# Kernel tuning notes

Hardware: AMD Instinct MI355X
Metric: run time of the kernel (lower is better)

Reference implementation:

```python
import jax, jax.numpy as jnp
import numpy as np

EPS = 1e-12  # torch F.normalize default eps


def _l2_normalize(x):
    # normalize along last dim, matching F.normalize(dim=2)
    norm = jnp.linalg.norm(x, axis=-1, keepdims=True)
    return x / jnp.maximum(norm, EPS)


def _poly_kernel_mean(a, b):
    # mean over (B,C,C) of squared inner products along T.
    # Original does broadcast (B,1,C,T)*(B,C,1,T) then sum; einsum is the
    # efficient batched-matmul form of the same math.
    g = jnp.einsum('bct,bdt->bcd', a, b)  # (B,C,C)
    return jnp.mean(g * g)


def setup_inputs() -> dict:
    key = jax.random.key(0)
    k1, k2 = jax.random.split(key)
    B, C, T = 16, 128, 16384
    f_s = jax.random.normal(k1, (B, C, T), dtype=jnp.float32)
    f_t = jax.random.normal(k2, (B, C, T), dtype=jnp.float32)
    return {"f_s": f_s, "f_t": f_t}


def reference(f_s, f_t):
    # equal T -> no interpolation branch; view(B,C,-1) is identity for 3D
    s = _l2_normalize(f_s)
    t = _l2_normalize(f_t)
    loss = (jax.lax.stop_gradient(_poly_kernel_mean(t, t))
            + _poly_kernel_mean(s, s)
            - 2.0 * _poly_kernel_mean(s, t))
    return loss
```

## Files before the change

kernel.cpp:

```cpp
#include <hip/hip_runtime.h>
#include <hip/hip_bf16.h>

#define BATCH  16
#define CCH    128
#define TDIM   16384
#define MROWS  256
#define NCHUNK 16
#define KC     (TDIM / NCHUNK)
#define BK     32
#define NSTEP  (KC / BK)
#define LDSP   40
#define GRAM   (MROWS * MROWS)

#define WS_NORMS 0
#define WS_DIAG  4096
#define WS_BODY  (4096 + 65536)

typedef __attribute__((ext_vector_type(8))) short bf16x8;
typedef __attribute__((ext_vector_type(4))) float f32x4;
typedef __attribute__((ext_vector_type(8))) unsigned short u16x8;

__device__ __forceinline__ unsigned short f2bf(float x) {
  unsigned int u = __float_as_uint(x);
  u += 0x7fffu + ((u >> 16) & 1u);
  return (unsigned short)(u >> 16);
}

__global__ __launch_bounds__(512, 2) void gram_kernel(
    const float* __restrict__ fs, const float* __restrict__ ft,
    float* __restrict__ outp, float* __restrict__ diagp, int atomic_mode)
{
  __shared__ __attribute__((aligned(16))) unsigned short sm[2][MROWS][LDSP];

  const int tid   = threadIdx.x;
  const int bidx  = blockIdx.x;
  const int b     = bidx / NCHUNK;
  const int chunk = bidx - b * NCHUNK;
  const int kbase = chunk * KC;

  const int lane = tid & 63;
  const int w    = tid >> 6;
  const int wr   = w & 3;
  const int wc   = w >> 2;
  const int lhi  = lane >> 4;
  const int llo  = lane & 15;
  const int koff = lhi * 8;

  const int srow = tid >> 1;
  const int half = tid & 1;
  const float* rp = ((srow < CCH)
      ? (fs + (size_t)(b * CCH + srow) * TDIM)
      : (ft + (size_t)(b * CCH + (srow - CCH)) * TDIM))
      + kbase + half * 16;

  f32x4 acc[4][8];
  #pragma unroll
  for (int i = 0; i < 4; ++i)
    #pragma unroll
    for (int j = 0; j < 8; ++j)
      acc[i][j] = (f32x4){0.f, 0.f, 0.f, 0.f};

  {
    f32x4 v0 = *(const f32x4*)(rp + 0);
    f32x4 v1 = *(const f32x4*)(rp + 4);
    f32x4 v2 = *(const f32x4*)(rp + 8);
    f32x4 v3 = *(const f32x4*)(rp + 12);
    u16x8 pa, pb;
    pa[0]=f2bf(v0.x); pa[1]=f2bf(v0.y); pa[2]=f2bf(v0.z); pa[3]=f2bf(v0.w);
    pa[4]=f2bf(v1.x); pa[5]=f2bf(v1.y); pa[6]=f2bf(v1.z); pa[7]=f2bf(v1.w);
    pb[0]=f2bf(v2.x); pb[1]=f2bf(v2.y); pb[2]=f2bf(v2.z); pb[3]=f2bf(v2.w);
    pb[4]=f2bf(v3.x); pb[5]=f2bf(v3.y); pb[6]=f2bf(v3.z); pb[7]=f2bf(v3.w);
    *(u16x8*)&sm[0][srow][half * 16]     = pa;
    *(u16x8*)&sm[0][srow][half * 16 + 8] = pb;
  }
  f32x4 p[2][4];
  #pragma unroll
  for (int k = 0; k < 4; ++k)
    p[1][k] = *(const f32x4*)(rp + 1 * BK + k * 4);
  __syncthreads();

  #pragma unroll 2
  for (int s = 0; s < NSTEP; ++s) {
    const int par = s & 1;
    if (s + 2 < NSTEP) {
      #pragma unroll
      for (int k = 0; k < 4; ++k)
        p[par][k] = *(const f32x4*)(rp + (s + 2) * BK + k * 4);
    }
    {
      bf16x8 af[4], bfr[8];
      #pragma unroll
      for (int i = 0; i < 4; ++i)
        af[i] = *(const bf16x8*)&sm[par][wr * 64 + i * 16 + llo][koff];
      #pragma unroll
      for (int j = 0; j < 8; ++j)
        bfr[j] = *(const bf16x8*)&sm[par][wc * 128 + j * 16 + llo][koff];
      #pragma unroll
      for (int i = 0; i < 4; ++i)
        #pragma unroll
        for (int j = 0; j < 8; ++j)
          acc[i][j] = __builtin_amdgcn_mfma_f32_16x16x32_bf16(af[i], bfr[j], acc[i][j], 0, 0, 0);
    }
    if (s + 1 < NSTEP) {
      u16x8 pa, pb;
      pa[0]=f2bf(p[par^1][0].x); pa[1]=f2bf(p[par^1][0].y); pa[2]=f2bf(p[par^1][0].z); pa[3]=f2bf(p[par^1][0].w);
      pa[4]=f2bf(p[par^1][1].x); pa[5]=f2bf(p[par^1][1].y); pa[6]=f2bf(p[par^1][1].z); pa[7]=f2bf(p[par^1][1].w);
      pb[0]=f2bf(p[par^1][2].x); pb[1]=f2bf(p[par^1][2].y); pb[2]=f2bf(p[par^1][2].z); pb[3]=f2bf(p[par^1][2].w);
      pb[4]=f2bf(p[par^1][3].x); pb[5]=f2bf(p[par^1][3].y); pb[6]=f2bf(p[par^1][3].z); pb[7]=f2bf(p[par^1][3].w);
      *(u16x8*)&sm[par ^ 1][srow][half * 16]     = pa;
      *(u16x8*)&sm[par ^ 1][srow][half * 16 + 8] = pb;
    }
    __syncthreads();
  }

  if (atomic_mode) {
    float* out = outp + (size_t)b * GRAM;
    #pragma unroll
    for (int i = 0; i < 4; ++i) {
      int row0 = wr * 64 + i * 16 + lhi * 4;
      #pragma unroll
      for (int j = 0; j < 8; ++j) {
        int col = wc * 128 + j * 16 + llo;
        #pragma unroll
        for (int r = 0; r < 4; ++r)
          atomicAdd(&out[(size_t)(row0 + r) * MROWS + col], acc[i][j][r]);
      }
    }
    if ((wr >> 1) == wc && (llo >> 2) == lhi) {
      #pragma unroll
      for (int i = 0; i < 4; ++i) {
        float dv = (wr & 1) ? acc[i][4 + i][llo & 3] : acc[i][i][llo & 3];
        atomicAdd(&diagp[b * MROWS + wr * 64 + i * 16 + llo], dv);
      }
    }
  } else {
    float* out = outp + (size_t)bidx * GRAM;
    #pragma unroll
    for (int i = 0; i < 4; ++i) {
      int row0 = wr * 64 + i * 16 + lhi * 4;
      #pragma unroll
      for (int j = 0; j < 8; ++j) {
        int col = wc * 128 + j * 16 + llo;
        #pragma unroll
        for (int r = 0; r < 4; ++r)
          out[(size_t)(row0 + r) * MROWS + col] = acc[i][j][r];
      }
    }
    if ((wr >> 1) == wc && (llo >> 2) == lhi) {
      #pragma unroll
      for (int i = 0; i < 4; ++i) {
        float dv = (wr & 1) ? acc[i][4 + i][llo & 3] : acc[i][i][llo & 3];
        diagp[bidx * MROWS + wr * 64 + i * 16 + llo] = dv;
      }
    }
  }
}

__global__ __launch_bounds__(256) void norms_kernel(
    const float* __restrict__ diagp, float* __restrict__ norms, int nchunk)
{
  int b = blockIdx.x;
  int d = threadIdx.x;
  float g = 0.f;
  for (int c = 0; c < nchunk; ++c)
    g += diagp[(b * nchunk + c) * MROWS + d];
  float n = sqrtf(fmaxf(g, 0.f));
  n = fmaxf(n, 1e-12f);
  norms[b * MROWS + d] = 1.0f / n;
}

__global__ __launch_bounds__(256) void loss_kernel(
    const float* __restrict__ body, const float* __restrict__ norms,
    float* __restrict__ out, int nchunk)
{
  int flat = blockIdx.x * 1024 + threadIdx.x * 4;
  int b    = flat >> 16;
  int e    = flat & 65535;
  const float* nb = norms + b * MROWS;

  f32x4 g = (f32x4){0.f, 0.f, 0.f, 0.f};
  const float* src = body + (size_t)b * nchunk * GRAM + e;
  #pragma unroll 4
  for (int c = 0; c < nchunk; ++c) {
    f32x4 v = *(const f32x4*)(src + (size_t)c * GRAM);
    g.x += v.x; g.y += v.y; g.z += v.z; g.w += v.w;
  }
  int i  = e >> 8;
  int j0 = e & 255;
  float ri = nb[i];
  f32x4 rj = *(const f32x4*)(nb + j0);
  float si = (i < CCH) ? 1.f : -1.f;
  float accl = 0.f;
  #pragma unroll
  for (int q = 0; q < 4; ++q) {
    int j = j0 + q;
    float gh = g[q] * ri * rj[q];
    float sgn = ((j < CCH) ? 1.f : -1.f) * si;
    accl += sgn * gh * gh;
  }
  #pragma unroll
  for (int off = 32; off > 0; off >>= 1)
    accl += __shfl_down(accl, off, 64);
  __shared__ float red[4];
  if ((threadIdx.x & 63) == 0) red[threadIdx.x >> 6] = accl;
  __syncthreads();
  if (threadIdx.x == 0) {
    float t = red[0] + red[1] + red[2] + red[3];
    atomicAdd(out, t * (1.0f / (float)(BATCH * CCH * CCH)));
  }
}

extern "C" void kernel_launch(void* const* d_in, const int* in_sizes, int n_in,
                              void* d_out, int out_size, void* d_ws, size_t ws_size,
                              hipStream_t stream) {
  const float* fs = (const float*)d_in[0];
  const float* ft = (const float*)d_in[1];
  float* out   = (float*)d_out;
  float* wsf   = (float*)d_ws;
  float* norms = wsf + WS_NORMS;
  float* diagp = wsf + WS_DIAG;
  float* body  = wsf + WS_BODY;

  const size_t need_partials =
      (size_t)(WS_BODY + (size_t)BATCH * NCHUNK * GRAM) * sizeof(float);
  const int atomic_mode = (ws_size >= need_partials) ? 0 : 1;
  const int nchunk = atomic_mode ? 1 : NCHUNK;

  (void)hipMemsetAsync(d_out, 0, sizeof(float), stream);
  if (atomic_mode) {
    (void)hipMemsetAsync(diagp, 0,
        (size_t)(65536 + (size_t)BATCH * GRAM) * sizeof(float), stream);
  }

  gram_kernel<<<dim3(BATCH * NCHUNK), dim3(512), 0, stream>>>(fs, ft, body, diagp, atomic_mode);
  norms_kernel<<<dim3(BATCH), dim3(256), 0, stream>>>(diagp, norms, nchunk);
  loss_kernel<<<dim3(1024), dim3(256), 0, stream>>>(body, norms, out, nchunk);
}
```

Measured before the change: 332.4 us.

## Triple-buffer LDS staging with two global loads in flight in gram kernel

Replaces the double-buffered K loop with a three-stage pipeline: three LDS buffers and three register staging sets. This lets two future K-steps' global loads be outstanding while the current step's MFMAs run. The loop is manually rotated over the three buffers, with an explicit tail and one barrier per step. The B-fragment loads are also split into two halves to lower peak register use. The aim is to hide HBM latency, since there is only one block per CU. The cost is more LDS per block and extra staging registers, which could spill or limit residency.

```diff
diff --git a/kernel.cpp b/kernel.cpp
--- a/kernel.cpp
+++ b/kernel.cpp
@@ -30,7 +30,7 @@
     const float* __restrict__ fs, const float* __restrict__ ft,
     float* __restrict__ outp, float* __restrict__ diagp, int atomic_mode)
 {
-  __shared__ __attribute__((aligned(16))) unsigned short sm[2][MROWS][LDSP];
+  __shared__ __attribute__((aligned(16))) unsigned short sm[3][MROWS][LDSP];
 
   const int tid   = threadIdx.x;
   const int bidx  = blockIdx.x;
@@ -60,58 +60,69 @@
     for (int j = 0; j < 8; ++j)
       acc[i][j] = (f32x4){0.f, 0.f, 0.f, 0.f};
 
-  {
-    f32x4 v0 = *(const f32x4*)(rp + 0);
-    f32x4 v1 = *(const f32x4*)(rp + 4);
-    f32x4 v2 = *(const f32x4*)(rp + 8);
-    f32x4 v3 = *(const f32x4*)(rp + 12);
-    u16x8 pa, pb;
-    pa[0]=f2bf(v0.x); pa[1]=f2bf(v0.y); pa[2]=f2bf(v0.z); pa[3]=f2bf(v0.w);
-    pa[4]=f2bf(v1.x); pa[5]=f2bf(v1.y); pa[6]=f2bf(v1.z); pa[7]=f2bf(v1.w);
-    pb[0]=f2bf(v2.x); pb[1]=f2bf(v2.y); pb[2]=f2bf(v2.z); pb[3]=f2bf(v2.w);
-    pb[4]=f2bf(v3.x); pb[5]=f2bf(v3.y); pb[6]=f2bf(v3.z); pb[7]=f2bf(v3.w);
-    *(u16x8*)&sm[0][srow][half * 16]     = pa;
-    *(u16x8*)&sm[0][srow][half * 16 + 8] = pb;
-  }
-  f32x4 p[2][4];
-  #pragma unroll
-  for (int k = 0; k < 4; ++k)
-    p[1][k] = *(const f32x4*)(rp + 1 * BK + k * 4);
+  f32x4 g0[4], g1[4], g2[4];
+
+#define ISSUE1(G, P) do {                       \
+    const float* _p = (P);                      \
+    G[0] = *(const f32x4*)(_p);                 \
+    G[1] = *(const f32x4*)(_p + 4);             \
+    G[2] = *(const f32x4*)(_p + 8);             \
+    G[3] = *(const f32x4*)(_p + 12);            \
+  } while (0)
+
+#define WRITE1(WB, G) do {                                                   \
+    u16x8 pa, pb;                                                            \
+    pa[0]=f2bf(G[0].x); pa[1]=f2bf(G[0].y); pa[2]=f2bf(G[0].z); pa[3]=f2bf(G[0].w); \
+    pa[4]=f2bf(G[1].x); pa[5]=f2bf(G[1].y); pa[6]=f2bf(G[1].z); pa[7]=f2bf(G[1].w); \
+    pb[0]=f2bf(G[2].x); pb[1]=f2bf(G[2].y); pb[2]=f2bf(G[2].z); pb[3]=f2bf(G[2].w); \
+    pb[4]=f2bf(G[3].x); pb[5]=f2bf(G[3].y); pb[6]=f2bf(G[3].z); pb[7]=f2bf(G[3].w); \
+    *(u16x8*)&sm[WB][srow][half * 16]     = pa;                              \
+    *(u16x8*)&sm[WB][srow][half * 16 + 8] = pb;                              \
+  } while (0)
+
+#define COMPUTE(C) do {                                                      \
+    bf16x8 af[4];                                                            \
+    _Pragma("unroll")                                                        \
+    for (int i = 0; i < 4; ++i)                                              \
+      af[i] = *(const bf16x8*)&sm[C][wr * 64 + i * 16 + llo][koff];          \
+    _Pragma("unroll")                                                        \
+    for (int jh = 0; jh < 2; ++jh) {                                         \
+      bf16x8 bq[4];                                                          \
+      _Pragma("unroll")                                                      \
+      for (int j = 0; j < 4; ++j)                                            \
+        bq[j] = *(const bf16x8*)&sm[C][wc * 128 + jh * 64 + j * 16 + llo][koff]; \
+      _Pragma("unroll")                                                      \
+      for (int i = 0; i < 4; ++i)                                            \
+        _Pragma("unroll")                                                    \
+        for (int j = 0; j < 4; ++j)                                          \
+          acc[i][jh * 4 + j] = __builtin_amdgcn_mfma_f32_16x16x32_bf16(      \
+              af[i], bq[j], acc[i][jh * 4 + j], 0, 0, 0);                    \
+    }                                                                        \
+  } while (0)
+
+  ISSUE1(g0, rp);
+  WRITE1(0, g0);
+  ISSUE1(g1, rp + BK);
+  ISSUE1(g2, rp + 2 * BK);
   __syncthreads();
 
-  #pragma unroll 2
-  for (int s = 0; s < NSTEP; ++s) {
-    const int par = s & 1;
-    if (s + 2 < NSTEP) {
-      #pragma unroll
-      for (int k = 0; k < 4; ++k)
-        p[par][k] = *(const f32x4*)(rp + (s + 2) * BK + k * 4);
-    }
-    {
-      bf16x8 af[4], bfr[8];
-      #pragma unroll
-      for (int i = 0; i < 4; ++i)
-        af[i] = *(const bf16x8*)&sm[par][wr * 64 + i * 16 + llo][koff];
-      #pragma unroll
-      for (int j = 0; j < 8; ++j)
-        bfr[j] = *(const bf16x8*)&sm[par][wc * 128 + j * 16 + llo][koff];
-      #pragma unroll
-      for (int i = 0; i < 4; ++i)
-        #pragma unroll
-        for (int j = 0; j < 8; ++j)
-          acc[i][j] = __builtin_amdgcn_mfma_f32_16x16x32_bf16(af[i], bfr[j], acc[i][j], 0, 0, 0);
-    }
-    if (s + 1 < NSTEP) {
-      u16x8 pa, pb;
-      pa[0]=f2bf(p[par^1][0].x); pa[1]=f2bf(p[par^1][0].y); pa[2]=f2bf(p[par^1][0].z); pa[3]=f2bf(p[par^1][0].w);
-      pa[4]=f2bf(p[par^1][1].x); pa[5]=f2bf(p[par^1][1].y); pa[6]=f2bf(p[par^1][1].z); pa[7]=f2bf(p[par^1][1].w);
-      pb[0]=f2bf(p[par^1][2].x); pb[1]=f2bf(p[par^1][2].y); pb[2]=f2bf(p[par^1][2].z); pb[3]=f2bf(p[par^1][2].w);
-      pb[4]=f2bf(p[par^1][3].x); pb[5]=f2bf(p[par^1][3].y); pb[6]=f2bf(p[par^1][3].z); pb[7]=f2bf(p[par^1][3].w);
-      *(u16x8*)&sm[par ^ 1][srow][half * 16]     = pa;
-      *(u16x8*)&sm[par ^ 1][srow][half * 16 + 8] = pb;
-    }
-    __syncthreads();
-  }
+  const float* rpi = rp + 3 * BK;
+  #pragma unroll 1
+  for (int t = 0; t < 9; ++t) {
+    ISSUE1(g0, rpi);           WRITE1(1, g1); COMPUTE(0); __syncthreads();
+    ISSUE1(g1, rpi + BK);      WRITE1(2, g2); COMPUTE(1); __syncthreads();
+    ISSUE1(g2, rpi + 2 * BK);  WRITE1(0, g0); COMPUTE(2); __syncthreads();
+    rpi += 3 * BK;
+  }
+  ISSUE1(g0, rpi);           WRITE1(1, g1); COMPUTE(0); __syncthreads();
+  ISSUE1(g1, rpi + BK);      WRITE1(2, g2); COMPUTE(1); __syncthreads();
+  WRITE1(0, g0);             COMPUTE(2);                __syncthreads();
+  WRITE1(1, g1);             COMPUTE(0);                __syncthreads();
+  COMPUTE(1);
+
+#undef ISSUE1
+#undef WRITE1
+#undef COMPUTE
 
   if (atomic_mode) {
     float* out = outp + (size_t)b * GRAM;
```

After: 343.1 us. 3.2% more time.
